# Optimization experiments

Measured on AMD Instinct MI355X. Metric: run time of the kernel, lower is better.

The kernel has to match this reference:

```python
import jax, jax.numpy as jnp
import numpy as np

B = 16384      # batch (rollout size)
OBS = 64       # obs_dim
ACT = 8        # action_dim
H = 128        # hidden_dim
NN = 4         # num_neighbors
N = NN + 1     # num_nodes in local graph
HEADS = 2
SLOPE = 0.2    # leaky_relu negative slope


def setup_inputs() -> dict:
    key = jax.random.key(0)
    ks = jax.random.split(key, 20)

    def glorot(k, shape):
        fan_in, fan_out = shape[0], shape[-1]
        lim = np.sqrt(6.0 / (fan_in + fan_out)).astype(np.float32)
        return jax.random.uniform(k, shape, jnp.float32, -lim, lim)

    obs = jax.random.normal(ks[0], (B, OBS), jnp.float32)
    neighbor_obs = jax.random.normal(ks[1], (B, NN, OBS), jnp.float32)
    adj = jax.random.randint(ks[2], (B, N), 0, 2, jnp.int32)
    adj = adj.at[:, 0].set(1)  # self node always connected (avoids all -inf rows)

    params = dict(
        enc_w1=glorot(ks[3], (OBS, H)), enc_b1=jnp.zeros((H,), jnp.float32),
        enc_w2=glorot(ks[4], (H, H)),  enc_b2=jnp.zeros((H,), jnp.float32),
        gat_w=glorot(ks[5], (HEADS, H, H)),       # per-head W (no bias)
        gat_a=glorot(ks[6], (HEADS, 2 * H)),      # per-head attention vector a
        val_w1=glorot(ks[7], (H * HEADS, H)), val_b1=jnp.zeros((H,), jnp.float32),
        val_w2=glorot(ks[8], (H, 1)),          val_b2=jnp.zeros((1,), jnp.float32),
        pol_w1=glorot(ks[9], (H * HEADS, H)), pol_b1=jnp.zeros((H,), jnp.float32),
        pol_w2=glorot(ks[10], (H, ACT)),       pol_b2=jnp.zeros((ACT,), jnp.float32),
    )
    return {"obs": obs, "neighbor_obs": neighbor_obs, "adj": adj, **params}


def reference(obs, neighbor_obs, adj,
              enc_w1, enc_b1, enc_w2, enc_b2,
              gat_w, gat_a,
              val_w1, val_b1, val_w2, val_b2,
              pol_w1, pol_b1, pol_w2, pol_b2):
    # shared local encoder applied to self obs and each neighbor obs
    all_obs = jnp.concatenate([obs[:, None, :], neighbor_obs], axis=1)   # [B,N,OBS]
    emb = jax.nn.relu(all_obs @ enc_w1 + enc_b1) @ enc_w2 + enc_b2       # [B,N,H]

    # GAT layer (all heads vectorized). Concat attention a^T[Wh_i||Wh_j]
    # decomposes into a1.Wh_i + a2.Wh_j.
    Wh = jnp.einsum('bnd,hdo->bhno', emb, gat_w)                          # [B,heads,N,H]
    a1, a2 = gat_a[:, :H], gat_a[:, H:]
    ei = jnp.einsum('bhno,ho->bhn', Wh, a1)                               # [B,heads,N]
    ej = jnp.einsum('bhno,ho->bhn', Wh, a2)
    e = jax.nn.leaky_relu(ei[..., :, None] + ej[..., None, :], SLOPE)     # [B,heads,N,N]
    # torch masked_fill broadcasts adj [B,N] as a column mask over j
    e = jnp.where((adj == 0)[:, None, None, :], -jnp.inf, e)
    attn = jax.nn.softmax(e, axis=-1)                                     # [B,heads,N,N]
    h_prime = jnp.einsum('bhij,bhjo->bhio', attn, Wh)                     # [B,heads,N,H]

    # node 0 (the agent itself), heads concatenated (head-major order, as torch cat)
    final = h_prime[:, :, 0, :].reshape(h_prime.shape[0], HEADS * H)      # [B,heads*H]

    value = jax.nn.relu(final @ val_w1 + val_b1) @ val_w2 + val_b2        # [B,1]
    logits = jax.nn.relu(final @ pol_w1 + pol_b1) @ pol_w2 + pol_b2      # [B,ACT]
    return value, logits
```

## Files before the change

kernel.cpp:

```cpp
#include <hip/hip_runtime.h>
#include <hip/hip_bf16.h>

#define B_TOT 16384
#define OBS 64
#define ACT 8
#define H 128
#define NNODE 5
#define HEADS 2
#define TB 16
#define ROWS (TB*NNODE)

typedef __attribute__((ext_vector_type(8))) short short8;
typedef __attribute__((ext_vector_type(4))) short short4v;
typedef __attribute__((ext_vector_type(4))) float f32x4;

__device__ __forceinline__ float bf2f(short s){
  unsigned int u = ((unsigned int)(unsigned short)s) << 16;
  return __uint_as_float(u);
}
__device__ __forceinline__ short f2bf(float f){
  __hip_bfloat16 h = __float2bfloat16(f);
  return *reinterpret_cast<short*>(&h);
}

#define LDS_X     0
#define LDS_H1    10240
#define LDS_WH    0
#define LDS_EMB   30720
#define LDS_FINAL 51200
#define LDS_V1    59392
#define LDS_P1    63488
#define LDS_EI0   67584
#define LDS_EJ    67648
#define LDS_ATT   67968
#define LDS_TOT   68352

template<int STRIDE>
__device__ __forceinline__ char* sw(char* base, int r, int k){
  int b = r*(STRIDE*2) + k*2;
  return base + (b ^ ((r & 7) << 4));
}

#define W_W1T  0
#define W_W2T  8192
#define W_GWT  24576
#define W_VW1T 57344
#define W_PW1T 90112
#define W_TOTAL 122880

__global__ void prep_weights(const float* __restrict__ enc_w1, const float* __restrict__ enc_w2,
                             const float* __restrict__ gat_w, const float* __restrict__ val_w1,
                             const float* __restrict__ pol_w1, unsigned short* __restrict__ wt){
  int t = blockIdx.x * 256 + threadIdx.x;
  float v;
  if (t < 8192){
    int c = t >> 6, k = t & 63;
    v = enc_w1[k*H + c];
  } else if (t < 24576){
    int u = t - 8192; int c = u >> 7, k = u & 127;
    v = enc_w2[k*H + c];
  } else if (t < 57344){
    int u = t - 24576; int h = u >> 14; int r = u & 16383;
    int c = r >> 7, k = r & 127;
    v = gat_w[h*16384 + k*H + c];
  } else if (t < 90112){
    int u = t - 57344; int c = u >> 8, k = u & 255;
    v = val_w1[k*H + c];
  } else {
    int u = t - 90112; int c = u >> 8, k = u & 255;
    v = pol_w1[k*H + c];
  }
  __hip_bfloat16 hv = __float2bfloat16(v);
  wt[t] = *reinterpret_cast<unsigned short*>(&hv);
}

template<int K, bool RELU, bool HASBIAS>
__device__ __forceinline__ void gemm80(char* lds, int a_off, const unsigned short* __restrict__ wt,
                                       const float* __restrict__ bias, int o_off, int lane, int wave){
  constexpr int KS = K / 32;
  const int lm = lane & 15;
  const int kb = (lane >> 4) * 8;
  const int c0 = wave*32 + lm;
  const int c1 = c0 + 16;
  short8 bf0[KS], bf1[KS];
  #pragma unroll
  for (int s = 0; s < KS; ++s){
    bf0[s] = *reinterpret_cast<const short8*>(wt + c0*K + s*32 + kb);
    bf1[s] = *reinterpret_cast<const short8*>(wt + c1*K + s*32 + kb);
  }
  const float bias0 = HASBIAS ? bias[c0] : 0.f;
  const float bias1 = HASBIAS ? bias[c1] : 0.f;
  #pragma unroll
  for (int mt = 0; mt < 5; ++mt){
    f32x4 acc0 = {0.f,0.f,0.f,0.f}, acc1 = {0.f,0.f,0.f,0.f};
    #pragma unroll
    for (int s = 0; s < KS; ++s){
      short8 a = *reinterpret_cast<short8*>(sw<K>(lds + a_off, mt*16 + lm, s*32 + kb));
      acc0 = __builtin_amdgcn_mfma_f32_16x16x32_bf16(a, bf0[s], acc0, 0, 0, 0);
      acc1 = __builtin_amdgcn_mfma_f32_16x16x32_bf16(a, bf1[s], acc1, 0, 0, 0);
    }
    const int r0 = mt*16 + ((lane >> 4) << 2);
    #pragma unroll
    for (int j = 0; j < 4; ++j){
      float v0 = acc0[j] + bias0;
      float v1 = acc1[j] + bias1;
      if (RELU){ v0 = fmaxf(v0, 0.f); v1 = fmaxf(v1, 0.f); }
      *reinterpret_cast<short*>(sw<H>(lds + o_off, r0 + j, c0)) = f2bf(v0);
      *reinterpret_cast<short*>(sw<H>(lds + o_off, r0 + j, c1)) = f2bf(v1);
    }
  }
}

__device__ __forceinline__ void gemm16(char* lds, const unsigned short* __restrict__ wt,
                                       const float* __restrict__ bias, int o_off, int lane, int wave){
  const int lm = lane & 15;
  const int kb = (lane >> 4) * 8;
  const int c0 = wave*32 + lm;
  const int c1 = c0 + 16;
  f32x4 acc0 = {0.f,0.f,0.f,0.f}, acc1 = {0.f,0.f,0.f,0.f};
  #pragma unroll
  for (int s = 0; s < 8; ++s){
    short8 a  = *reinterpret_cast<short8*>(sw<256>(lds + LDS_FINAL, lm, s*32 + kb));
    short8 b0 = *reinterpret_cast<const short8*>(wt + c0*256 + s*32 + kb);
    short8 b1 = *reinterpret_cast<const short8*>(wt + c1*256 + s*32 + kb);
    acc0 = __builtin_amdgcn_mfma_f32_16x16x32_bf16(a, b0, acc0, 0, 0, 0);
    acc1 = __builtin_amdgcn_mfma_f32_16x16x32_bf16(a, b1, acc1, 0, 0, 0);
  }
  const int r0 = (lane >> 4) << 2;
  #pragma unroll
  for (int j = 0; j < 4; ++j){
    float v0 = fmaxf(acc0[j] + bias[c0], 0.f);
    float v1 = fmaxf(acc1[j] + bias[c1], 0.f);
    *reinterpret_cast<short*>(sw<H>(lds + o_off, r0 + j, c0)) = f2bf(v0);
    *reinterpret_cast<short*>(sw<H>(lds + o_off, r0 + j, c1)) = f2bf(v1);
  }
}

__global__ __launch_bounds__(256, 2) void colight_main(
    const float* __restrict__ obs, const float* __restrict__ nobs, const int* __restrict__ adj,
    const float* __restrict__ enc_b1, const float* __restrict__ enc_b2,
    const float* __restrict__ gat_a,
    const float* __restrict__ val_b1, const float* __restrict__ val_w2, const float* __restrict__ val_b2,
    const float* __restrict__ pol_b1, const float* __restrict__ pol_w2, const float* __restrict__ pol_b2,
    const unsigned short* __restrict__ wt_all,
    float* __restrict__ dout)
{
  __shared__ __align__(16) char lds[LDS_TOT];
  const int tid  = threadIdx.x;
  const int lane = tid & 63;
  const int wave = tid >> 6;
  const int b0   = blockIdx.x * TB;

  const unsigned short* w1t  = wt_all + W_W1T;
  const unsigned short* w2t  = wt_all + W_W2T;
  const unsigned short* gwt  = wt_all + W_GWT;
  const unsigned short* vw1t = wt_all + W_VW1T;
  const unsigned short* pw1t = wt_all + W_PW1T;

  #pragma unroll
  for (int i = 0; i < 5; ++i){
    int chunk = tid + i*256;
    int row = chunk >> 4;
    int c4  = (chunk & 15) * 4;
    int lb  = row / 5;
    int n   = row - lb*5;
    const float* src = (n == 0) ? (obs  + (size_t)(b0 + lb)*OBS + c4)
                                : (nobs + ((size_t)(b0 + lb)*4 + (n-1))*OBS + c4);
    float4 v = *reinterpret_cast<const float4*>(src);
    short4v p = { f2bf(v.x), f2bf(v.y), f2bf(v.z), f2bf(v.w) };
    *reinterpret_cast<short4v*>(sw<OBS>(lds + LDS_X, row, c4)) = p;
  }
  __syncthreads();

  gemm80<64, true, true>(lds, LDS_X, w1t, enc_b1, LDS_H1, lane, wave);
  __syncthreads();
  gemm80<128, false, true>(lds, LDS_H1, w2t, enc_b2, LDS_EMB, lane, wave);
  __syncthreads();

  float* ei0 = reinterpret_cast<float*>(lds + LDS_EI0);
  float* ej  = reinterpret_cast<float*>(lds + LDS_EJ);
  float* att = reinterpret_cast<float*>(lds + LDS_ATT);

  for (int h = 0; h < HEADS; ++h){
    gemm80<128, false, false>(lds, LDS_EMB, gwt + h*16384, nullptr, LDS_WH, lane, wave);
    __syncthreads();

    if (tid < 192){
      const int isei = (tid >= 160);
      const int q    = isei ? (tid - 160) : tid;
      const int row  = isei ? ((q >> 1) * 5) : (q >> 1);
      const int half = q & 1;
      const float* av = gat_a + h*2*H + (isei ? 0 : H);
      float s = 0.f;
      #pragma unroll
      for (int i = 0; i < 8; ++i){
        short8 v = *reinterpret_cast<short8*>(sw<H>(lds + LDS_WH, row, half*64 + i*8));
        #pragma unroll
        for (int e = 0; e < 8; ++e) s += bf2f(v[e]) * av[half*64 + i*8 + e];
      }
      s += __shfl_xor(s, 1);
      if (!half){ if (isei) ei0[q >> 1] = s; else ej[q >> 1] = s; }
    }
    __syncthreads();

    if (tid < TB){
      const int lb = tid;
      const float e0 = ei0[lb];
      float p[NNODE]; int msk[NNODE];
      float m = -1e30f;
      #pragma unroll
      for (int j = 0; j < NNODE; ++j){
        msk[j] = adj[(size_t)(b0 + lb)*NNODE + j];
        float s = e0 + ej[lb*NNODE + j];
        s = (s > 0.f) ? s : 0.2f * s;
        p[j] = s;
        if (msk[j] && s > m) m = s;
      }
      float den = 0.f;
      #pragma unroll
      for (int j = 0; j < NNODE; ++j){
        float e = msk[j] ? __expf(p[j] - m) : 0.f;
        p[j] = e; den += e;
      }
      const float inv = 1.f / den;
      #pragma unroll
      for (int j = 0; j < NNODE; ++j) att[lb*NNODE + j] = p[j] * inv;
    }
    __syncthreads();

    {
      const int lb = tid >> 4;
      const int cg = tid & 15;
      float acc[8] = {0,0,0,0,0,0,0,0};
      #pragma unroll
      for (int j = 0; j < NNODE; ++j){
        const float aj = att[lb*NNODE + j];
        short8 v = *reinterpret_cast<short8*>(sw<H>(lds + LDS_WH, lb*NNODE + j, cg*8));
        #pragma unroll
        for (int e = 0; e < 8; ++e) acc[e] += aj * bf2f(v[e]);
      }
      short8 o;
      #pragma unroll
      for (int e = 0; e < 8; ++e) o[e] = f2bf(acc[e]);
      *reinterpret_cast<short8*>(sw<HEADS*H>(lds + LDS_FINAL, lb, h*H + cg*8)) = o;
    }
    __syncthreads();
  }

  gemm16(lds, vw1t, val_b1, LDS_V1, lane, wave);
  gemm16(lds, pw1t, pol_b1, LDS_P1, lane, wave);
  __syncthreads();

  if (tid < 128){
    const int lb = tid >> 3, a = tid & 7;
    float s = pol_b2[a];
    #pragma unroll
    for (int i = 0; i < 16; ++i){
      short8 v = *reinterpret_cast<short8*>(sw<H>(lds + LDS_P1, lb, i*8));
      #pragma unroll
      for (int e = 0; e < 8; ++e) s += bf2f(v[e]) * pol_w2[(i*8 + e)*ACT + a];
    }
    dout[B_TOT + (size_t)(b0 + lb)*ACT + a] = s;
  } else if (tid < 160){
    const int q = tid - 128;
    const int lb = q >> 1, half = q & 1;
    float s = 0.f;
    #pragma unroll
    for (int i = 0; i < 8; ++i){
      short8 v = *reinterpret_cast<short8*>(sw<H>(lds + LDS_V1, lb, half*64 + i*8));
      #pragma unroll
      for (int e = 0; e < 8; ++e) s += bf2f(v[e]) * val_w2[half*64 + i*8 + e];
    }
    s += __shfl_xor(s, 1);
    if (!half) dout[b0 + lb] = s + val_b2[0];
  }
}

extern "C" void kernel_launch(void* const* d_in, const int* in_sizes, int n_in,
                              void* d_out, int out_size, void* d_ws, size_t ws_size,
                              hipStream_t stream) {
  (void)in_sizes; (void)n_in; (void)out_size; (void)ws_size;
  const float* obs    = (const float*)d_in[0];
  const float* nobs   = (const float*)d_in[1];
  const int*   adj    = (const int*)  d_in[2];
  const float* enc_w1 = (const float*)d_in[3];
  const float* enc_b1 = (const float*)d_in[4];
  const float* enc_w2 = (const float*)d_in[5];
  const float* enc_b2 = (const float*)d_in[6];
  const float* gat_w  = (const float*)d_in[7];
  const float* gat_a  = (const float*)d_in[8];
  const float* val_w1 = (const float*)d_in[9];
  const float* val_b1 = (const float*)d_in[10];
  const float* val_w2 = (const float*)d_in[11];
  const float* val_b2 = (const float*)d_in[12];
  const float* pol_w1 = (const float*)d_in[13];
  const float* pol_b1 = (const float*)d_in[14];
  const float* pol_w2 = (const float*)d_in[15];
  const float* pol_b2 = (const float*)d_in[16];

  unsigned short* wt = (unsigned short*)d_ws;

  prep_weights<<<W_TOTAL/256, 256, 0, stream>>>(enc_w1, enc_w2, gat_w, val_w1, pol_w1, wt);

  colight_main<<<B_TOT/TB, 256, 0, stream>>>(
      obs, nobs, adj, enc_b1, enc_b2, gat_a,
      val_b1, val_w2, val_b2, pol_b1, pol_w2, pol_b2,
      wt, (float*)d_out);
}
```

Measured before the change: 142.1 us.

## Restructure fused GAT kernel into per-wave agent tiles with register-resident attention

Each wave now handles 4 agents (20 rows, padded to 32) on its own: encoder, GAT projection, attention scores, softmax and aggregation all stay in registers or a private LDS slice. Block-wide barriers are replaced by wave-local lgkmcnt fences, which cuts LDS traffic and synchronisation. The value and policy first layers are merged into one 256-wide GEMM, and the second-layer weights are pre-cast to bf16. The cost is MFMA work spent on padding rows (32 computed for 20 used), heavier register pressure from the 2x8 accumulator tile, and reloading the weights from global memory in every wave.

```diff
diff --git a/kernel.cpp b/kernel.cpp
--- a/kernel.cpp
+++ b/kernel.cpp
@@ -2,277 +2,333 @@
 #include <hip/hip_bf16.h>
 
 #define B_TOT 16384
-#define OBS 64
-#define ACT 8
-#define H 128
-#define NNODE 5
-#define HEADS 2
-#define TB 16
-#define ROWS (TB*NNODE)
 
 typedef __attribute__((ext_vector_type(8))) short short8;
 typedef __attribute__((ext_vector_type(4))) short short4v;
 typedef __attribute__((ext_vector_type(4))) float f32x4;
 
 __device__ __forceinline__ float bf2f(short s){
-  unsigned int u = ((unsigned int)(unsigned short)s) << 16;
+  unsigned u = ((unsigned)(unsigned short)s) << 16;
   return __uint_as_float(u);
+}
+__device__ __forceinline__ unsigned f2bfu(float f){
+  __hip_bfloat16 h = __float2bfloat16(f);
+  return (unsigned)*reinterpret_cast<unsigned short*>(&h);
 }
 __device__ __forceinline__ short f2bf(float f){
   __hip_bfloat16 h = __float2bfloat16(f);
   return *reinterpret_cast<short*>(&h);
 }
-
-#define LDS_X     0
-#define LDS_H1    10240
-#define LDS_WH    0
-#define LDS_EMB   30720
-#define LDS_FINAL 51200
-#define LDS_V1    59392
-#define LDS_P1    63488
-#define LDS_EI0   67584
-#define LDS_EJ    67648
-#define LDS_ATT   67968
-#define LDS_TOT   68352
-
-template<int STRIDE>
-__device__ __forceinline__ char* sw(char* base, int r, int k){
-  int b = r*(STRIDE*2) + k*2;
-  return base + (b ^ ((r & 7) << 4));
-}
-
-#define W_W1T  0
-#define W_W2T  8192
-#define W_GWT  24576
-#define W_VW1T 57344
-#define W_PW1T 90112
-#define W_TOTAL 122880
+__device__ __forceinline__ void wave_fence(){
+  asm volatile("s_waitcnt lgkmcnt(0)" ::: "memory");
+  __builtin_amdgcn_sched_barrier(0);
+}
+
+#define W_W1T   0
+#define W_W2T   8192
+#define W_GWT   24576
+#define W_HW1T  57344
+#define W_PW2T  122880
+#define W_VW2   123904
+#define W_TOTAL 124032
 
 __global__ void prep_weights(const float* __restrict__ enc_w1, const float* __restrict__ enc_w2,
                              const float* __restrict__ gat_w, const float* __restrict__ val_w1,
-                             const float* __restrict__ pol_w1, unsigned short* __restrict__ wt){
-  int t = blockIdx.x * 256 + threadIdx.x;
+                             const float* __restrict__ pol_w1, const float* __restrict__ pol_w2,
+                             const float* __restrict__ val_w2, unsigned short* __restrict__ wt){
+  int t = blockIdx.x*256 + threadIdx.x;
+  if (t >= W_TOTAL) return;
   float v;
-  if (t < 8192){
-    int c = t >> 6, k = t & 63;
-    v = enc_w1[k*H + c];
-  } else if (t < 24576){
-    int u = t - 8192; int c = u >> 7, k = u & 127;
-    v = enc_w2[k*H + c];
-  } else if (t < 57344){
-    int u = t - 24576; int h = u >> 14; int r = u & 16383;
-    int c = r >> 7, k = r & 127;
-    v = gat_w[h*16384 + k*H + c];
-  } else if (t < 90112){
-    int u = t - 57344; int c = u >> 8, k = u & 255;
-    v = val_w1[k*H + c];
-  } else {
-    int u = t - 90112; int c = u >> 8, k = u & 255;
-    v = pol_w1[k*H + c];
-  }
-  __hip_bfloat16 hv = __float2bfloat16(v);
-  wt[t] = *reinterpret_cast<unsigned short*>(&hv);
-}
-
-template<int K, bool RELU, bool HASBIAS>
-__device__ __forceinline__ void gemm80(char* lds, int a_off, const unsigned short* __restrict__ wt,
-                                       const float* __restrict__ bias, int o_off, int lane, int wave){
-  constexpr int KS = K / 32;
-  const int lm = lane & 15;
-  const int kb = (lane >> 4) * 8;
-  const int c0 = wave*32 + lm;
-  const int c1 = c0 + 16;
-  short8 bf0[KS], bf1[KS];
-  #pragma unroll
-  for (int s = 0; s < KS; ++s){
-    bf0[s] = *reinterpret_cast<const short8*>(wt + c0*K + s*32 + kb);
-    bf1[s] = *reinterpret_cast<const short8*>(wt + c1*K + s*32 + kb);
-  }
-  const float bias0 = HASBIAS ? bias[c0] : 0.f;
-  const float bias1 = HASBIAS ? bias[c1] : 0.f;
-  #pragma unroll
-  for (int mt = 0; mt < 5; ++mt){
-    f32x4 acc0 = {0.f,0.f,0.f,0.f}, acc1 = {0.f,0.f,0.f,0.f};
-    #pragma unroll
-    for (int s = 0; s < KS; ++s){
-      short8 a = *reinterpret_cast<short8*>(sw<K>(lds + a_off, mt*16 + lm, s*32 + kb));
-      acc0 = __builtin_amdgcn_mfma_f32_16x16x32_bf16(a, bf0[s], acc0, 0, 0, 0);
-      acc1 = __builtin_amdgcn_mfma_f32_16x16x32_bf16(a, bf1[s], acc1, 0, 0, 0);
-    }
-    const int r0 = mt*16 + ((lane >> 4) << 2);
-    #pragma unroll
-    for (int j = 0; j < 4; ++j){
-      float v0 = acc0[j] + bias0;
-      float v1 = acc1[j] + bias1;
-      if (RELU){ v0 = fmaxf(v0, 0.f); v1 = fmaxf(v1, 0.f); }
-      *reinterpret_cast<short*>(sw<H>(lds + o_off, r0 + j, c0)) = f2bf(v0);
-      *reinterpret_cast<short*>(sw<H>(lds + o_off, r0 + j, c1)) = f2bf(v1);
-    }
-  }
-}
-
-__device__ __forceinline__ void gemm16(char* lds, const unsigned short* __restrict__ wt,
-                                       const float* __restrict__ bias, int o_off, int lane, int wave){
-  const int lm = lane & 15;
-  const int kb = (lane >> 4) * 8;
-  const int c0 = wave*32 + lm;
-  const int c1 = c0 + 16;
-  f32x4 acc0 = {0.f,0.f,0.f,0.f}, acc1 = {0.f,0.f,0.f,0.f};
-  #pragma unroll
-  for (int s = 0; s < 8; ++s){
-    short8 a  = *reinterpret_cast<short8*>(sw<256>(lds + LDS_FINAL, lm, s*32 + kb));
-    short8 b0 = *reinterpret_cast<const short8*>(wt + c0*256 + s*32 + kb);
-    short8 b1 = *reinterpret_cast<const short8*>(wt + c1*256 + s*32 + kb);
-    acc0 = __builtin_amdgcn_mfma_f32_16x16x32_bf16(a, b0, acc0, 0, 0, 0);
-    acc1 = __builtin_amdgcn_mfma_f32_16x16x32_bf16(a, b1, acc1, 0, 0, 0);
-  }
-  const int r0 = (lane >> 4) << 2;
-  #pragma unroll
-  for (int j = 0; j < 4; ++j){
-    float v0 = fmaxf(acc0[j] + bias[c0], 0.f);
-    float v1 = fmaxf(acc1[j] + bias[c1], 0.f);
-    *reinterpret_cast<short*>(sw<H>(lds + o_off, r0 + j, c0)) = f2bf(v0);
-    *reinterpret_cast<short*>(sw<H>(lds + o_off, r0 + j, c1)) = f2bf(v1);
-  }
-}
+  if (t < 8192){ int c=t>>6, k=t&63; v = enc_w1[k*128 + c]; }
+  else if (t < 24576){ int u=t-8192, c=u>>7, k=u&127; v = enc_w2[k*128 + c]; }
+  else if (t < 57344){ int u=t-24576, h=u>>14, r=u&16383, c=r>>7, k=r&127; v = gat_w[h*16384 + k*128 + c]; }
+  else if (t < 122880){ int u=t-57344, oc=u>>8, k=u&255; v = (oc<128) ? val_w1[k*128+oc] : pol_w1[k*128+(oc-128)]; }
+  else if (t < 123904){ int u=t-122880, a=u>>7, k=u&127; v = pol_w2[k*8+a]; }
+  else { int u=t-123904; v = val_w2[u]; }
+  wt[t] = (unsigned short)f2bfu(v);
+}
+
+#define WSTR      5632
+#define MISC_OFF  22528
+#define FINAL_OFF 23552
+#define LDS_TOT   31744
+
+#define MFMA16(a,b,c) __builtin_amdgcn_mfma_f32_16x16x32_bf16(a,b,c,0,0,0)
 
 __global__ __launch_bounds__(256, 2) void colight_main(
     const float* __restrict__ obs, const float* __restrict__ nobs, const int* __restrict__ adj,
     const float* __restrict__ enc_b1, const float* __restrict__ enc_b2,
     const float* __restrict__ gat_a,
-    const float* __restrict__ val_b1, const float* __restrict__ val_w2, const float* __restrict__ val_b2,
-    const float* __restrict__ pol_b1, const float* __restrict__ pol_w2, const float* __restrict__ pol_b2,
+    const float* __restrict__ val_b1, const float* __restrict__ val_b2,
+    const float* __restrict__ pol_b1, const float* __restrict__ pol_b2,
     const unsigned short* __restrict__ wt_all,
     float* __restrict__ dout)
 {
   __shared__ __align__(16) char lds[LDS_TOT];
   const int tid  = threadIdx.x;
   const int lane = tid & 63;
-  const int wave = tid >> 6;
-  const int b0   = blockIdx.x * TB;
+  const int wv   = tid >> 6;
+  const int lm   = lane & 15;
+  const int grp  = lane >> 4;
+  const int kb   = grp * 8;
+  const int gblk = blockIdx.x * 16;
+  const int gw   = gblk + wv*4;
+
+  char* ws = lds + wv*WSTR;
+  float* ejL  = reinterpret_cast<float*>(lds + MISC_OFF + wv*256);
+  float* ei0L = ejL + 20;
+  int*   adjL = reinterpret_cast<int*>(ejL + 24);
 
   const unsigned short* w1t  = wt_all + W_W1T;
   const unsigned short* w2t  = wt_all + W_W2T;
   const unsigned short* gwt  = wt_all + W_GWT;
-  const unsigned short* vw1t = wt_all + W_VW1T;
-  const unsigned short* pw1t = wt_all + W_PW1T;
-
+  const unsigned short* hw1t = wt_all + W_HW1T;
+  const unsigned short* pw2t = wt_all + W_PW2T;
+  const unsigned short* vw2  = wt_all + W_VW2;
+
+
+  if (lane < 20) adjL[lane] = adj[(gw + lane/5)*5 + (lane%5)];
   #pragma unroll
   for (int i = 0; i < 5; ++i){
-    int chunk = tid + i*256;
+    int chunk = i*64 + lane;
     int row = chunk >> 4;
     int c4  = (chunk & 15) * 4;
-    int lb  = row / 5;
-    int n   = row - lb*5;
-    const float* src = (n == 0) ? (obs  + (size_t)(b0 + lb)*OBS + c4)
-                                : (nobs + ((size_t)(b0 + lb)*4 + (n-1))*OBS + c4);
+    int a = row/5, n = row%5;
+    const float* src = n ? (nobs + ((gw+a)*4 + (n-1))*64 + c4)
+                         : (obs  + (gw+a)*64 + c4);
     float4 v = *reinterpret_cast<const float4*>(src);
     short4v p = { f2bf(v.x), f2bf(v.y), f2bf(v.z), f2bf(v.w) };
-    *reinterpret_cast<short4v*>(sw<OBS>(lds + LDS_X, row, c4)) = p;
+    *reinterpret_cast<short4v*>(ws + ((row*128 + c4*2) ^ ((row & 7) << 4))) = p;
+  }
+  wave_fence();
+
+  f32x4 acc[2][8];
+
+  #pragma unroll
+  for (int mt=0; mt<2; ++mt)
+    #pragma unroll
+    for (int nt=0; nt<8; ++nt) acc[mt][nt] = (f32x4){0.f,0.f,0.f,0.f};
+  #pragma unroll
+  for (int ks=0; ks<2; ++ks){
+    short8 xa0 = *reinterpret_cast<short8*>(ws + (((lm   )*128 + (ks*32+kb)*2) ^ ((lm&7)<<4)));
+    short8 xa1 = *reinterpret_cast<short8*>(ws + (((16+lm)*128 + (ks*32+kb)*2) ^ ((lm&7)<<4)));
+    #pragma unroll
+    for (int nt=0; nt<8; ++nt){
+      short8 b = *reinterpret_cast<const short8*>(w1t + (nt*16+lm)*64 + ks*32 + kb);
+      acc[0][nt] = MFMA16(xa0, b, acc[0][nt]);
+      acc[1][nt] = MFMA16(xa1, b, acc[1][nt]);
+    }
+  }
+  {
+    float bv[8];
+    #pragma unroll
+    for (int nt=0; nt<8; ++nt) bv[nt] = enc_b1[nt*16+lm];
+    wave_fence();
+    #pragma unroll
+    for (int mt=0; mt<2; ++mt)
+      #pragma unroll
+      for (int nt=0; nt<8; ++nt)
+        #pragma unroll
+        for (int j=0; j<4; ++j){
+          int row = mt*16 + grp*4 + j;
+          if (row < 20)
+            *reinterpret_cast<short*>(ws + ((row*256 + (nt*16+lm)*2) ^ ((row&7)<<4)))
+              = f2bf(fmaxf(acc[mt][nt][j] + bv[nt], 0.f));
+        }
+  }
+  wave_fence();
+
+  #pragma unroll
+  for (int mt=0; mt<2; ++mt)
+    #pragma unroll
+    for (int nt=0; nt<8; ++nt) acc[mt][nt] = (f32x4){0.f,0.f,0.f,0.f};
+  #pragma unroll
+  for (int kf=0; kf<4; ++kf){
+    short8 ha0 = *reinterpret_cast<short8*>(ws + (((lm   )*256 + (kf*32+kb)*2) ^ ((lm&7)<<4)));
+    short8 ha1 = *reinterpret_cast<short8*>(ws + (((16+lm)*256 + (kf*32+kb)*2) ^ ((lm&7)<<4)));
+    #pragma unroll
+    for (int nt=0; nt<8; ++nt){
+      short8 b = *reinterpret_cast<const short8*>(w2t + (nt*16+lm)*128 + kf*32 + kb);
+      acc[0][nt] = MFMA16(ha0, b, acc[0][nt]);
+      acc[1][nt] = MFMA16(ha1, b, acc[1][nt]);
+    }
+  }
+  {
+    float bv[8];
+    #pragma unroll
+    for (int nt=0; nt<8; ++nt) bv[nt] = enc_b2[nt*16+lm];
+    wave_fence();
+    #pragma unroll
+    for (int mt=0; mt<2; ++mt)
+      #pragma unroll
+      for (int nt=0; nt<8; ++nt)
+        #pragma unroll
+        for (int j=0; j<4; ++j){
+          int row = mt*16 + grp*4 + j;
+          if (row < 20)
+            *reinterpret_cast<short*>(ws + ((row*256 + (nt*16+lm)*2) ^ ((row&7)<<4)))
+              = f2bf(acc[mt][nt][j] + bv[nt]);
+        }
+  }
+  wave_fence();
+
+  unsigned fin[2][4][4];
+  #pragma unroll
+  for (int h=0; h<2; ++h){
+    #pragma unroll
+    for (int mt=0; mt<2; ++mt)
+      #pragma unroll
+      for (int nt=0; nt<8; ++nt) acc[mt][nt] = (f32x4){0.f,0.f,0.f,0.f};
+    #pragma unroll
+    for (int kf=0; kf<4; ++kf){
+      short8 ea0 = *reinterpret_cast<short8*>(ws + (((lm   )*256 + (kf*32+kb)*2) ^ ((lm&7)<<4)));
+      short8 ea1 = *reinterpret_cast<short8*>(ws + (((16+lm)*256 + (kf*32+kb)*2) ^ ((lm&7)<<4)));
+      #pragma unroll
+      for (int nt=0; nt<8; ++nt){
+        short8 b = *reinterpret_cast<const short8*>(gwt + h*16384 + (nt*16+lm)*128 + kf*32 + kb);
+        acc[0][nt] = MFMA16(ea0, b, acc[0][nt]);
+        acc[1][nt] = MFMA16(ea1, b, acc[1][nt]);
+      }
+    }
+    {
+      float a1v[8], a2v[8];
+      #pragma unroll
+      for (int nt=0; nt<8; ++nt){
+        a1v[nt] = gat_a[h*256 + nt*16 + lm];
+        a2v[nt] = gat_a[h*256 + 128 + nt*16 + lm];
+      }
+      #pragma unroll
+      for (int mt=0; mt<2; ++mt)
+        #pragma unroll
+        for (int j=0; j<4; ++j){
+          float s1 = 0.f, s2 = 0.f;
+          #pragma unroll
+          for (int nt=0; nt<8; ++nt){ s1 += acc[mt][nt][j]*a1v[nt]; s2 += acc[mt][nt][j]*a2v[nt]; }
+          s1 += __shfl_xor(s1,1); s1 += __shfl_xor(s1,2); s1 += __shfl_xor(s1,4); s1 += __shfl_xor(s1,8);
+          s2 += __shfl_xor(s2,1); s2 += __shfl_xor(s2,2); s2 += __shfl_xor(s2,4); s2 += __shfl_xor(s2,8);
+          int row = mt*16 + grp*4 + j;
+          if (lm == 0 && row < 20){
+            ejL[row] = s2;
+            if (row % 5 == 0) ei0L[row/5] = s1;
+          }
+        }
+    }
+    wave_fence();
+    float att[5];
+    {
+      int a_ = lane & 3;
+      float e0 = ei0L[a_];
+      int msk[5]; float mx = -1e30f;
+      #pragma unroll
+      for (int n=0; n<5; ++n){
+        msk[n] = adjL[a_*5 + n];
+        float s = e0 + ejL[a_*5 + n];
+        s = (s > 0.f) ? s : 0.2f*s;
+        att[n] = s;
+        if (msk[n] && s > mx) mx = s;
+      }
+      float den = 0.f;
+      #pragma unroll
+      for (int n=0; n<5; ++n){
+        float e = msk[n] ? __expf(att[n]-mx) : 0.f;
+        att[n] = e; den += e;
+      }
+      float inv = 1.f/den;
+      #pragma unroll
+      for (int n=0; n<5; ++n) att[n] *= inv;
+    }
+    #pragma unroll
+    for (int ag=0; ag<4; ++ag){
+      float s[8];
+      #pragma unroll
+      for (int nt=0; nt<8; ++nt) s[nt] = 0.f;
+      #pragma unroll
+      for (int n=0; n<5; ++n){
+        const int r = ag*5 + n, mt = r >> 4, g2 = (r >> 2) & 3, j = r & 3;
+        float wn = __shfl(att[n], ag);
+        #pragma unroll
+        for (int nt=0; nt<8; ++nt){
+          float t = (grp == g2) ? wn*acc[mt][nt][j] : 0.f;
+          s[nt] += t;
+        }
+      }
+      #pragma unroll
+      for (int nt=0; nt<8; ++nt){ s[nt] += __shfl_xor(s[nt],16); s[nt] += __shfl_xor(s[nt],32); }
+      #pragma unroll
+      for (int p=0; p<4; ++p)
+        fin[h][ag][p] = f2bfu(s[2*p]) | (f2bfu(s[2*p+1]) << 16);
+    }
+  }
+
+  if (lane < 32){
+    #pragma unroll
+    for (int ag=0; ag<4; ++ag)
+      #pragma unroll
+      for (int p=0; p<4; ++p){
+        unsigned v = (lane < 16) ? fin[0][ag][p] : fin[1][ag][p];
+        int rowA = wv*4 + ag;
+        int c0 = ((lane < 16) ? 0 : 128) + 2*p*16 + lm;
+        *reinterpret_cast<short*>(lds + FINAL_OFF + ((rowA*512 + c0*2) ^ ((rowA&7)<<4)))
+            = (short)(v & 0xffff);
+        *reinterpret_cast<short*>(lds + FINAL_OFF + ((rowA*512 + (c0+16)*2) ^ ((rowA&7)<<4)))
+            = (short)(v >> 16);
+      }
   }
   __syncthreads();
 
-  gemm80<64, true, true>(lds, LDS_X, w1t, enc_b1, LDS_H1, lane, wave);
+
+  {
+    short8 fa[8];
+    #pragma unroll
+    for (int kf=0; kf<8; ++kf)
+      fa[kf] = *reinterpret_cast<short8*>(lds + FINAL_OFF + ((lm*512 + (kf*32+kb)*2) ^ ((lm&7)<<4)));
+    f32x4 hacc[4];
+    #pragma unroll
+    for (int nt=0; nt<4; ++nt) hacc[nt] = (f32x4){0.f,0.f,0.f,0.f};
+    #pragma unroll
+    for (int kf=0; kf<8; ++kf)
+      #pragma unroll
+      for (int nt=0; nt<4; ++nt){
+        short8 b = *reinterpret_cast<const short8*>(hw1t + (wv*64 + nt*16+lm)*256 + kf*32 + kb);
+        hacc[nt] = MFMA16(fa[kf], b, hacc[nt]);
+      }
+    #pragma unroll
+    for (int nt=0; nt<4; ++nt){
+      int oc = wv*64 + nt*16 + lm;
+      float bv = (oc < 128) ? val_b1[oc] : pol_b1[oc-128];
+      #pragma unroll
+      for (int j=0; j<4; ++j){
+        int row = grp*4 + j;
+        *reinterpret_cast<short*>(lds + ((row*512 + oc*2) ^ ((row&7)<<4)))
+            = f2bf(fmaxf(hacc[nt][j] + bv, 0.f));
+      }
+    }
+  }
   __syncthreads();
-  gemm80<128, false, true>(lds, LDS_H1, w2t, enc_b2, LDS_EMB, lane, wave);
-  __syncthreads();
-
-  float* ei0 = reinterpret_cast<float*>(lds + LDS_EI0);
-  float* ej  = reinterpret_cast<float*>(lds + LDS_EJ);
-  float* att = reinterpret_cast<float*>(lds + LDS_ATT);
-
-  for (int h = 0; h < HEADS; ++h){
-    gemm80<128, false, false>(lds, LDS_EMB, gwt + h*16384, nullptr, LDS_WH, lane, wave);
-    __syncthreads();
-
-    if (tid < 192){
-      const int isei = (tid >= 160);
-      const int q    = isei ? (tid - 160) : tid;
-      const int row  = isei ? ((q >> 1) * 5) : (q >> 1);
-      const int half = q & 1;
-      const float* av = gat_a + h*2*H + (isei ? 0 : H);
-      float s = 0.f;
-      #pragma unroll
-      for (int i = 0; i < 8; ++i){
-        short8 v = *reinterpret_cast<short8*>(sw<H>(lds + LDS_WH, row, half*64 + i*8));
-        #pragma unroll
-        for (int e = 0; e < 8; ++e) s += bf2f(v[e]) * av[half*64 + i*8 + e];
-      }
-      s += __shfl_xor(s, 1);
-      if (!half){ if (isei) ei0[q >> 1] = s; else ej[q >> 1] = s; }
-    }
-    __syncthreads();
-
-    if (tid < TB){
-      const int lb = tid;
-      const float e0 = ei0[lb];
-      float p[NNODE]; int msk[NNODE];
-      float m = -1e30f;
-      #pragma unroll
-      for (int j = 0; j < NNODE; ++j){
-        msk[j] = adj[(size_t)(b0 + lb)*NNODE + j];
-        float s = e0 + ej[lb*NNODE + j];
-        s = (s > 0.f) ? s : 0.2f * s;
-        p[j] = s;
-        if (msk[j] && s > m) m = s;
-      }
-      float den = 0.f;
-      #pragma unroll
-      for (int j = 0; j < NNODE; ++j){
-        float e = msk[j] ? __expf(p[j] - m) : 0.f;
-        p[j] = e; den += e;
-      }
-      const float inv = 1.f / den;
-      #pragma unroll
-      for (int j = 0; j < NNODE; ++j) att[lb*NNODE + j] = p[j] * inv;
-    }
-    __syncthreads();
-
-    {
-      const int lb = tid >> 4;
-      const int cg = tid & 15;
-      float acc[8] = {0,0,0,0,0,0,0,0};
-      #pragma unroll
-      for (int j = 0; j < NNODE; ++j){
-        const float aj = att[lb*NNODE + j];
-        short8 v = *reinterpret_cast<short8*>(sw<H>(lds + LDS_WH, lb*NNODE + j, cg*8));
-        #pragma unroll
-        for (int e = 0; e < 8; ++e) acc[e] += aj * bf2f(v[e]);
-      }
-      short8 o;
-      #pragma unroll
-      for (int e = 0; e < 8; ++e) o[e] = f2bf(acc[e]);
-      *reinterpret_cast<short8*>(sw<HEADS*H>(lds + LDS_FINAL, lb, h*H + cg*8)) = o;
-    }
-    __syncthreads();
-  }
-
-  gemm16(lds, vw1t, val_b1, LDS_V1, lane, wave);
-  gemm16(lds, pw1t, pol_b1, LDS_P1, lane, wave);
-  __syncthreads();
 
   if (tid < 128){
-    const int lb = tid >> 3, a = tid & 7;
-    float s = pol_b2[a];
-    #pragma unroll
-    for (int i = 0; i < 16; ++i){
-      short8 v = *reinterpret_cast<short8*>(sw<H>(lds + LDS_P1, lb, i*8));
-      #pragma unroll
-      for (int e = 0; e < 8; ++e) s += bf2f(v[e]) * pol_w2[(i*8 + e)*ACT + a];
-    }
-    dout[B_TOT + (size_t)(b0 + lb)*ACT + a] = s;
+    int a = tid >> 3, act = tid & 7;
+    float s = pol_b2[act];
+    #pragma unroll
+    for (int i=0; i<16; ++i){
+      short8 v = *reinterpret_cast<short8*>(lds + ((a*512 + (128 + i*8)*2) ^ ((a&7)<<4)));
+      short8 w = *reinterpret_cast<const short8*>(pw2t + act*128 + i*8);
+      #pragma unroll
+      for (int e=0; e<8; ++e) s += bf2f(v[e]) * bf2f(w[e]);
+    }
+    dout[B_TOT + (gblk + a)*8 + act] = s;
   } else if (tid < 160){
-    const int q = tid - 128;
-    const int lb = q >> 1, half = q & 1;
+    int q = tid - 128, a = q >> 1, hf = q & 1;
     float s = 0.f;
     #pragma unroll
-    for (int i = 0; i < 8; ++i){
-      short8 v = *reinterpret_cast<short8*>(sw<H>(lds + LDS_V1, lb, half*64 + i*8));
-      #pragma unroll
-      for (int e = 0; e < 8; ++e) s += bf2f(v[e]) * val_w2[half*64 + i*8 + e];
+    for (int i=0; i<8; ++i){
+      short8 v = *reinterpret_cast<short8*>(lds + ((a*512 + (hf*64 + i*8)*2) ^ ((a&7)<<4)));
+      short8 w = *reinterpret_cast<const short8*>(vw2 + hf*64 + i*8);
+      #pragma unroll
+      for (int e=0; e<8; ++e) s += bf2f(v[e]) * bf2f(w[e]);
     }
     s += __shfl_xor(s, 1);
-    if (!half) dout[b0 + lb] = s + val_b2[0];
+    if (!hf) dout[gblk + a] = s + val_b2[0];
   }
 }
 
@@ -300,10 +356,11 @@
 
   unsigned short* wt = (unsigned short*)d_ws;
 
-  prep_weights<<<W_TOTAL/256, 256, 0, stream>>>(enc_w1, enc_w2, gat_w, val_w1, pol_w1, wt);
-
-  colight_main<<<B_TOT/TB, 256, 0, stream>>>(
+  prep_weights<<<(W_TOTAL+255)/256, 256, 0, stream>>>(enc_w1, enc_w2, gat_w, val_w1, pol_w1,
+                                                      pol_w2, val_w2, wt);
+
+  colight_main<<<B_TOT/16, 256, 0, stream>>>(
       obs, nobs, adj, enc_b1, enc_b2, gat_a,
-      val_b1, val_w2, val_b2, pol_b1, pol_w2, pol_b2,
+      val_b1, val_b2, pol_b1, pol_b2,
       wt, (float*)d_out);
 }
```

Result: slower. 184.1 us (+29.6%).
